# Kernel optimization log

Measured on AMD Instinct MI355X. Metric: run time of the kernel, lower is better.

The kernel has to match this reference:

```python
import jax, jax.numpy as jnp
import numpy as np

N_NODES = 50000
N_EDGES = 800000
IN_DIM = 256
HID = [256, 128]
NEG_SLOPE = 0.01  # F.leaky_relu default


def setup_inputs() -> dict:
    key = jax.random.key(0)
    ks = jax.random.split(key, 8)
    x = jax.random.normal(ks[0], (N_NODES, IN_DIM), dtype=jnp.float32)
    w1 = jax.random.normal(ks[1], (IN_DIM, HID[0]), dtype=jnp.float32) * (1.0 / np.sqrt(IN_DIM))
    b1 = jnp.zeros((HID[0],), dtype=jnp.float32)
    w2 = jax.random.normal(ks[2], (HID[0], HID[1]), dtype=jnp.float32) * (1.0 / np.sqrt(HID[0]))
    b2 = jnp.zeros((HID[1],), dtype=jnp.float32)
    src = jax.random.randint(ks[3], (N_EDGES,), 0, N_NODES, dtype=jnp.int32)
    dst = jax.random.randint(ks[4], (N_EDGES,), 0, N_NODES, dtype=jnp.int32)
    edge_weight = jax.random.uniform(ks[5], (N_EDGES,), dtype=jnp.float32)
    return {"x": x, "w1": w1, "b1": b1, "w2": w2, "b2": b2,
            "src": src, "dst": dst, "edge_weight": edge_weight}


def _gcn_layer(h, w, b, src, dst, ew, n_nodes):
    # GraphConvolution: support = h @ W ; out = spmm(adj, support) + b
    support = h @ w                              # [N, d_out]
    msg = support[src] * ew[:, None]             # [E, d_out] gather + scale
    agg = jax.ops.segment_sum(msg, dst, num_segments=n_nodes)  # [N, d_out]
    return agg + b


def reference(x, w1, b1, w2, b2, src, dst, edge_weight):
    # layer 1: GCN -> leaky_relu -> dropout(eval: identity)
    h = _gcn_layer(x, w1, b1, src, dst, edge_weight, N_NODES)
    h = jax.nn.leaky_relu(h, NEG_SLOPE)
    # layer 2
    h = _gcn_layer(h, w2, b2, src, dst, edge_weight, N_NODES)
    h = jax.nn.leaky_relu(h, NEG_SLOPE)
    return h
```

## Files before the change

kernel.cpp:

```cpp
#include <hip/hip_runtime.h>

#define NEG_SLOPE 0.01f

constexpr int N_NODES_C = 50000;
constexpr int N_EDGES_C = 800000;
constexpr int M_PAD = 50048;
constexpr int META_CAP = 950016;

typedef short bf16x8 __attribute__((ext_vector_type(8)));
typedef float f32x4 __attribute__((ext_vector_type(4)));

__device__ inline unsigned short f2bf(float f) {
  unsigned int u = __float_as_uint(f);
  u += 0x7FFF + ((u >> 16) & 1);
  return (unsigned short)(u >> 16);
}
__device__ inline float bf2f(unsigned int h16) {
  return __uint_as_float(h16 << 16);
}

constexpr int NB_CONVX = (M_PAD * 8) / 256;
constexpr int NB_W1 = (256 * 256) / 256;
constexpr int NB_W2 = (256 * 128) / 256;
constexpr int NB_HIST = ((N_EDGES_C / 4) + 255) / 256;
constexpr int NB_NONH = NB_CONVX + NB_W1 + NB_W2;
constexpr int NB_PRE = NB_NONH + NB_HIST;
constexpr int NB_IL = 2 * NB_HIST;

__global__ __launch_bounds__(256) void pre_kernel(
    const float* __restrict__ x, const float* __restrict__ w1,
    const float* __restrict__ w2, const int* __restrict__ dst,
    unsigned short* __restrict__ xb, unsigned short* __restrict__ w1T,
    unsigned short* __restrict__ w2T, int* __restrict__ counts) {
  const int bx = blockIdx.x;
  const int tid = threadIdx.x;
  int l = 0, isHist = 0, h = 0;
  if (bx < NB_IL) {
    if (bx & 1) { isHist = 1; h = bx >> 1; }
    else l = bx >> 1;
  } else {
    l = bx - NB_HIST;
  }

  if (isHist) {
    int e = (h * 256 + tid) * 4;
    if (e < N_EDGES_C) {
      int4 d4 = *(const int4*)(dst + e);
      atomicAdd(&counts[d4.x], 1);
      atomicAdd(&counts[d4.y], 1);
      atomicAdd(&counts[d4.z], 1);
      atomicAdd(&counts[d4.w], 1);
    }
  } else if (l < NB_CONVX) {
    int idx = l * 256 + tid;
    int row = idx >> 3;
    int c32 = (idx & 7) * 32;
    uint4 o[4];
    if (row < N_NODES_C) {
      const float4* p = (const float4*)(x + (size_t)row * 256 + c32);
      float4 f[8];
#pragma unroll
      for (int i = 0; i < 8; ++i) f[i] = p[i];
#pragma unroll
      for (int i = 0; i < 4; ++i) {
        o[i].x = f2bf(f[2 * i].x) | ((unsigned)f2bf(f[2 * i].y) << 16);
        o[i].y = f2bf(f[2 * i].z) | ((unsigned)f2bf(f[2 * i].w) << 16);
        o[i].z = f2bf(f[2 * i + 1].x) | ((unsigned)f2bf(f[2 * i + 1].y) << 16);
        o[i].w = f2bf(f[2 * i + 1].z) | ((unsigned)f2bf(f[2 * i + 1].w) << 16);
      }
    } else {
#pragma unroll
      for (int i = 0; i < 4; ++i) o[i] = make_uint4(0, 0, 0, 0);
    }
#pragma unroll
    for (int i = 0; i < 4; ++i)
      *(uint4*)(xb + (size_t)row * 256 + c32 + i * 8) = o[i];
  } else if (l < NB_CONVX + NB_W1) {
    int idx = (l - NB_CONVX) * 256 + tid;
    int n = idx >> 8, k = idx & 255;
    w1T[idx] = f2bf(w1[(size_t)k * 256 + n]);
  } else {
    int idx = (l - NB_CONVX - NB_W1) * 256 + tid;
    int n = idx >> 8, k = idx & 255;
    w2T[idx] = f2bf(w2[(size_t)k * 128 + n]);
  }
}

constexpr int NB_NODE = (N_NODES_C + 255) / 256;
constexpr int NB_SCAT = (M_PAD + 255) / 256;

__global__ __launch_bounds__(256) void hist_kernel(const int* __restrict__ counts,
                                                   int* __restrict__ hist2,
                                                   int* __restrict__ ehist) {
  __shared__ int lh[64], le[64];
  const int t = threadIdx.x;
  if (t < 64) { lh[t] = 0; le[t] = 0; }
  __syncthreads();
  const int i = blockIdx.x * 256 + t;
  if (i < N_NODES_C) {
    int d = counts[i];
    int bin = d < 63 ? d : 63;
    atomicAdd(&lh[bin], 1);
    atomicAdd(&le[bin], (d + 3) & ~3);
  }
  __syncthreads();
  if (t < 64) {
    if (lh[t]) atomicAdd(&hist2[t], lh[t]);
    if (le[t]) atomicAdd(&ehist[t], le[t]);
  }
}

__global__ __launch_bounds__(256) void scatter_kernel(
    const int* __restrict__ counts, const int* __restrict__ hist2,
    const int* __restrict__ ehist, int* __restrict__ gclaim_n,
    int* __restrict__ gclaim_e, int* __restrict__ perm,
    int* __restrict__ nstart, int* __restrict__ ndeg,
    int* __restrict__ cursor, unsigned* __restrict__ s_meta) {
  __shared__ int nbase[64], ebase[64], lh[64], le[64], gn[64], ge[64];
  const int t = threadIdx.x;
  if (t < 64) {
    int hv = hist2[t], ev = ehist[t];
    int xs = hv, xe = ev;
#pragma unroll
    for (int off = 1; off < 64; off <<= 1) {
      int a = __shfl_up(xs, off);
      int b = __shfl_up(xe, off);
      if (t >= off) { xs += a; xe += b; }
    }
    nbase[t] = xs - hv;
    ebase[t] = xe - ev;
    lh[t] = 0;
    le[t] = 0;
  }
  __syncthreads();
  const int idx = blockIdx.x * 256 + t;
  int d = -1, bin = 0, lrank = 0, erank = 0;
  if (idx < N_NODES_C) {
    d = counts[idx];
    bin = d < 63 ? d : 63;
    lrank = atomicAdd(&lh[bin], 1);
    erank = atomicAdd(&le[bin], (d + 3) & ~3);
  } else if (idx < M_PAD) {
    perm[idx] = idx;
    nstart[idx] = 0;
    ndeg[idx] = 0;
  }
  __syncthreads();
  if (t < 64) {
    gn[t] = lh[t] ? nbase[t] + atomicAdd(&gclaim_n[t], lh[t]) : 0;
    ge[t] = le[t] ? ebase[t] + atomicAdd(&gclaim_e[t], le[t]) : 0;
  }
  __syncthreads();
  if (d >= 0) {
    const int grank = gn[bin] + lrank;
    const int estart = ge[bin] + erank;
    perm[grank] = idx;
    nstart[grank] = estart;
    ndeg[grank] = d;
    cursor[idx] = estart;
    const int d4 = (d + 3) & ~3;
    for (int j = d; j < d4; ++j) s_meta[estart + j] = 0;
  }
}


#define GLOAD_LDS16(g, l)                                              \
  __builtin_amdgcn_global_load_lds(                                    \
      (__attribute__((address_space(1))) void*)(g),                    \
      (__attribute__((address_space(3))) void*)(l), 16, 0, 0)

__device__ __forceinline__ void gemm_tile(
    const unsigned short* __restrict__ A,
    const unsigned short* __restrict__ BT,
    unsigned short* __restrict__ C,
    int N, int row0, int col0, short* Asm, short* Bsm) {
  constexpr int K = 256;
  const int tid = threadIdx.x;
  const int lane = tid & 63, wave = tid >> 6;
  const int wm = wave & 1, wn = wave >> 1;

  const int ch0 = wave * 2, ch1 = wave * 2 + 1;
  const int o0 = ch0 * 512 + lane * 8;
  const int o1 = ch1 * 512 + lane * 8;
  const int r0 = o0 >> 5, c0 = o0 & 31;
  const int r1 = o1 >> 5, c1 = o1 & 31;

  f32x4 acc[4][4] = {};

  for (int k0 = 0; k0 < K; k0 += 32) {
    GLOAD_LDS16(A + (size_t)(row0 + r0) * K + k0 + c0, &Asm[ch0 * 512]);
    GLOAD_LDS16(A + (size_t)(row0 + r1) * K + k0 + c1, &Asm[ch1 * 512]);
    GLOAD_LDS16(BT + (size_t)(col0 + r0) * K + k0 + c0, &Bsm[ch0 * 512]);
    GLOAD_LDS16(BT + (size_t)(col0 + r1) * K + k0 + c1, &Bsm[ch1 * 512]);
    __builtin_amdgcn_s_waitcnt(0);
    __syncthreads();

    bf16x8 af[4], bf[4];
#pragma unroll
    for (int mt = 0; mt < 4; ++mt)
      af[mt] = *(const bf16x8*)&Asm[(wm * 64 + mt * 16 + (lane & 15)) * 32 + (lane >> 4) * 8];
#pragma unroll
    for (int nt = 0; nt < 4; ++nt)
      bf[nt] = *(const bf16x8*)&Bsm[(wn * 64 + nt * 16 + (lane & 15)) * 32 + (lane >> 4) * 8];
#pragma unroll
    for (int mt = 0; mt < 4; ++mt)
#pragma unroll
      for (int nt = 0; nt < 4; ++nt)
        acc[mt][nt] = __builtin_amdgcn_mfma_f32_16x16x32_bf16(af[mt], bf[nt], acc[mt][nt], 0, 0, 0);
    __syncthreads();
  }

  const int cl = lane & 15, rq = (lane >> 4) * 4;
#pragma unroll
  for (int mt = 0; mt < 4; ++mt) {
    const int rbase = row0 + wm * 64 + mt * 16 + rq;
#pragma unroll
    for (int nt = 0; nt < 4; ++nt) {
      const int col = col0 + wn * 64 + nt * 16 + cl;
      const size_t sbase = ((size_t)(col >> 5) * M_PAD) * 32 + (col & 31);
#pragma unroll
      for (int i = 0; i < 4; ++i)
        C[sbase + (size_t)(rbase + i) * 32] = f2bf(acc[mt][nt][i]);
    }
  }
}

constexpr int NB_GEMM1 = 2 * (M_PAD / 128);
constexpr int NB_FILL = ((N_EDGES_C / 4) + 255) / 256;

__global__ __launch_bounds__(256) void fill_gemm1_kernel(
    const unsigned short* __restrict__ A, const unsigned short* __restrict__ BT,
    unsigned short* __restrict__ C, const int* __restrict__ src,
    const int* __restrict__ dst, const float* __restrict__ ew,
    int* __restrict__ cursor, unsigned* __restrict__ s_meta) {
  __shared__ short Asm[128 * 32];
  __shared__ short Bsm[128 * 32];
  const int b = blockIdx.x;
  if ((b & 1) == 0) {
    const int t = b >> 1;
    gemm_tile(A, BT, C, 256, (t >> 1) * 128, (t & 1) * 128, Asm, Bsm);
  } else {
    const int g = (b >> 1) * 256 + threadIdx.x;
    const int e = g * 4;
    if (e < N_EDGES_C) {
      int4 d4 = *(const int4*)(dst + e);
      int4 s4 = *(const int4*)(src + e);
      float4 w4 = *(const float4*)(ew + e);
      unsigned m0 = (unsigned)s4.x | ((unsigned)f2bf(w4.x) << 16);
      unsigned m1 = (unsigned)s4.y | ((unsigned)f2bf(w4.y) << 16);
      unsigned m2 = (unsigned)s4.z | ((unsigned)f2bf(w4.z) << 16);
      unsigned m3 = (unsigned)s4.w | ((unsigned)f2bf(w4.w) << 16);
      int p0 = atomicAdd(&cursor[d4.x], 1);
      int p1 = atomicAdd(&cursor[d4.y], 1);
      int p2 = atomicAdd(&cursor[d4.z], 1);
      int p3 = atomicAdd(&cursor[d4.w], 1);
      __builtin_nontemporal_store(m0, s_meta + p0);
      __builtin_nontemporal_store(m1, s_meta + p1);
      __builtin_nontemporal_store(m2, s_meta + p2);
      __builtin_nontemporal_store(m3, s_meta + p3);
    }
  }
}

__global__ __launch_bounds__(256) void gemm2_kernel(
    const unsigned short* __restrict__ A, const unsigned short* __restrict__ BT,
    unsigned short* __restrict__ C) {
  __shared__ short Asm[128 * 32];
  __shared__ short Bsm[128 * 32];
  gemm_tile(A, BT, C, 128, blockIdx.x * 128, 0, Asm, Bsm);
}


__device__ inline void fma4(float* acc, uint2 v, float wt) {
  acc[0] += bf2f(v.x & 0xffffu) * wt;
  acc[1] += bf2f(v.x >> 16) * wt;
  acc[2] += bf2f(v.y & 0xffffu) * wt;
  acc[3] += bf2f(v.y >> 16) * wt;
}

__device__ __forceinline__ void gfma4h(float* acc, uint4 m,
                                       const unsigned short* __restrict__ tab,
                                       int dimg) {
  uint2 v0 = *(const uint2*)(tab + (m.x & 0xffffu) * 32 + dimg * 4);
  uint2 v1 = *(const uint2*)(tab + (m.y & 0xffffu) * 32 + dimg * 4);
  uint2 v2 = *(const uint2*)(tab + (m.z & 0xffffu) * 32 + dimg * 4);
  uint2 v3 = *(const uint2*)(tab + (m.w & 0xffffu) * 32 + dimg * 4);
  fma4(acc, v0, bf2f(m.x >> 16));
  fma4(acc, v1, bf2f(m.y >> 16));
  fma4(acc, v2, bf2f(m.z >> 16));
  fma4(acc, v3, bf2f(m.w >> 16));
}

template <int NSLICE, int OUT_D, bool OUT_BF16>
__global__ __launch_bounds__(256) void agg_lite_kernel(
    const unsigned short* __restrict__ supS,
    const unsigned* __restrict__ s_meta,
    const int* __restrict__ nstart, const int* __restrict__ ndeg,
    const int* __restrict__ perm, const float* __restrict__ bias,
    unsigned short* __restrict__ out_bf, float* __restrict__ out_f, int n_total) {
  const int bx = blockIdx.x;
  const int slice = bx & (NSLICE - 1);
  const int group = bx / NSLICE;
  const int tid = threadIdx.x;
  const int wv = tid >> 6;
  const int oct = (tid & 63) >> 3;
  const int dimg = tid & 7;
  const int idx = group * 32 + wv * 8 + oct;
  if (idx >= n_total) return;
  const int n = perm[idx];
  const bool valid = n < N_NODES_C;
  const unsigned short* tab = supS + (size_t)slice * M_PAD * 32;

  float acc[4] = {};
  const int s = nstart[idx];
  const int nq = (ndeg[idx] + 3) >> 2;
  const uint4* mp = (const uint4*)(s_meta + s);

  if (nq > 0) {
    uint4 m0 = mp[0];
    uint4 m1 = (nq > 1) ? mp[1] : make_uint4(0, 0, 0, 0);
    int q = 0;
    for (; q + 2 < nq; q += 2) {
      uint4 p0 = mp[q + 2];
      uint4 p1 = mp[q + 3];
      gfma4h(acc, m0, tab, dimg);
      gfma4h(acc, m1, tab, dimg);
      m0 = p0;
      m1 = p1;
    }
    gfma4h(acc, m0, tab, dimg);
    if (q + 1 < nq) gfma4h(acc, m1, tab, dimg);
  }

  const int dbase = slice * 32 + dimg * 4;
  if (OUT_BF16) {
    unsigned short o[4];
#pragma unroll
    for (int j = 0; j < 4; ++j) {
      if (valid) {
        float v = acc[j] + bias[dbase + j];
        v = v >= 0.f ? v : NEG_SLOPE * v;
        o[j] = f2bf(v);
      } else {
        o[j] = 0;
      }
    }
    uint2 pk;
    pk.x = o[0] | ((unsigned)o[1] << 16);
    pk.y = o[2] | ((unsigned)o[3] << 16);
    *(uint2*)(out_bf + (size_t)n * OUT_D + dbase) = pk;
  } else if (valid) {
    float r[4];
#pragma unroll
    for (int j = 0; j < 4; ++j) {
      float v = acc[j] + bias[dbase + j];
      r[j] = v >= 0.f ? v : NEG_SLOPE * v;
    }
    *(float4*)(out_f + (size_t)n * OUT_D + dbase) = make_float4(r[0], r[1], r[2], r[3]);
  }
}


extern "C" void kernel_launch(void* const* d_in, const int* in_sizes, int n_in,
                              void* d_out, int out_size, void* d_ws, size_t ws_size,
                              hipStream_t stream) {
  const float* x  = (const float*)d_in[0];
  const float* w1 = (const float*)d_in[1];
  const float* b1 = (const float*)d_in[2];
  const float* w2 = (const float*)d_in[3];
  const float* b2 = (const float*)d_in[4];
  const int*   src = (const int*)d_in[5];
  const int*   dst = (const int*)d_in[6];
  const float* ew  = (const float*)d_in[7];
  float* out = (float*)d_out;

  unsigned short* xb   = (unsigned short*)d_ws;
  unsigned short* a2b  = xb + (size_t)M_PAD * 256;
  unsigned short* sup1 = a2b + (size_t)M_PAD * 256;
  unsigned short* sup2 = sup1 + (size_t)M_PAD * 256;
  unsigned short* w1T  = sup2 + (size_t)M_PAD * 128;
  unsigned short* w2T  = w1T + 256 * 256;
  int* counts  = (int*)(w2T + 128 * 256);
  int* cursor  = counts + N_NODES_C;
  int* perm    = cursor + N_NODES_C;
  int* nstart  = perm + M_PAD;
  int* ndeg    = nstart + M_PAD;
  int* hist2   = ndeg + M_PAD;
  int* ehist   = hist2 + 64;
  int* gclaim_n= ehist + 64;
  int* gclaim_e= gclaim_n + 64;
  unsigned* s_meta = (unsigned*)(gclaim_e + 64);

  hipMemsetAsync(counts, 0, N_NODES_C * sizeof(int), stream);
  hipMemsetAsync(hist2, 0, 256 * sizeof(int), stream);
  pre_kernel<<<NB_PRE, 256, 0, stream>>>(x, w1, w2, dst, xb, w1T, w2T, counts);

  hist_kernel<<<NB_NODE, 256, 0, stream>>>(counts, hist2, ehist);
  scatter_kernel<<<NB_SCAT, 256, 0, stream>>>(counts, hist2, ehist, gclaim_n,
                                              gclaim_e, perm, nstart, ndeg,
                                              cursor, s_meta);

  fill_gemm1_kernel<<<NB_GEMM1 + NB_FILL, 256, 0, stream>>>(
      xb, w1T, sup1, src, dst, ew, cursor, s_meta);

  agg_lite_kernel<8, 256, true><<<(M_PAD / 32) * 8, 256, 0, stream>>>(
      sup1, s_meta, nstart, ndeg, perm, b1, a2b, nullptr, M_PAD);

  gemm2_kernel<<<M_PAD / 128, 256, 0, stream>>>(a2b, w2T, sup2);
  agg_lite_kernel<4, 128, false><<<((N_NODES_C + 31) / 32) * 4, 256, 0, stream>>>(
      sup2, s_meta, nstart, ndeg, perm, b2, nullptr, out, N_NODES_C);
}
```

Measured before the change: 284.6 us.

## Switch support to row-major and aggregate with one wave per node

The GEMM epilogues now write the support matrices row-major instead of as 32-column slice tables. The aggregation kernel is rewritten so each 64-lane wave owns one node and gathers whole neighbor rows, with each lane holding 4 columns (layer 1) or 2 columns (layer 2). This reads each node's edge metadata once instead of once per slice and makes every gathered row access wider and contiguous. In exchange it gives up the small per-slice working set that could stay resident in L2, since the gather now touches the full support table.

Result: slower. 296.1 us (+4.0%).

```diff
diff --git a/kernel.cpp b/kernel.cpp
--- a/kernel.cpp
+++ b/kernel.cpp
@@ -173,7 +173,7 @@
     const unsigned short* __restrict__ A,
     const unsigned short* __restrict__ BT,
     unsigned short* __restrict__ C,
-    int N, int row0, int col0, short* Asm, short* Bsm) {
+    int N, int ldc, int row0, int col0, short* Asm, short* Bsm) {
   constexpr int K = 256;
   const int tid = threadIdx.x;
   const int lane = tid & 63, wave = tid >> 6;
@@ -217,10 +217,9 @@
 #pragma unroll
     for (int nt = 0; nt < 4; ++nt) {
       const int col = col0 + wn * 64 + nt * 16 + cl;
-      const size_t sbase = ((size_t)(col >> 5) * M_PAD) * 32 + (col & 31);
 #pragma unroll
       for (int i = 0; i < 4; ++i)
-        C[sbase + (size_t)(rbase + i) * 32] = f2bf(acc[mt][nt][i]);
+        C[(size_t)(rbase + i) * ldc + col] = f2bf(acc[mt][nt][i]);
     }
   }
 }
@@ -238,7 +237,7 @@
   const int b = blockIdx.x;
   if ((b & 1) == 0) {
     const int t = b >> 1;
-    gemm_tile(A, BT, C, 256, (t >> 1) * 128, (t & 1) * 128, Asm, Bsm);
+    gemm_tile(A, BT, C, 256, 256, (t >> 1) * 128, (t & 1) * 128, Asm, Bsm);
   } else {
     const int g = (b >> 1) * 256 + threadIdx.x;
     const int e = g * 4;
@@ -267,54 +266,55 @@
     unsigned short* __restrict__ C) {
   __shared__ short Asm[128 * 32];
   __shared__ short Bsm[128 * 32];
-  gemm_tile(A, BT, C, 128, blockIdx.x * 128, 0, Asm, Bsm);
-}
-
-
-__device__ inline void fma4(float* acc, uint2 v, float wt) {
+  gemm_tile(A, BT, C, 128, 128, blockIdx.x * 128, 0, Asm, Bsm);
+}
+
+
+__device__ __forceinline__ void rfma_256(float* acc, unsigned m,
+                                         const unsigned short* __restrict__ tp) {
+  uint2 v = *(const uint2*)(tp + (size_t)(m & 0xffffu) * 256);
+  float wt = bf2f(m >> 16);
   acc[0] += bf2f(v.x & 0xffffu) * wt;
   acc[1] += bf2f(v.x >> 16) * wt;
   acc[2] += bf2f(v.y & 0xffffu) * wt;
   acc[3] += bf2f(v.y >> 16) * wt;
 }
 
-__device__ __forceinline__ void gfma4h(float* acc, uint4 m,
-                                       const unsigned short* __restrict__ tab,
-                                       int dimg) {
-  uint2 v0 = *(const uint2*)(tab + (m.x & 0xffffu) * 32 + dimg * 4);
-  uint2 v1 = *(const uint2*)(tab + (m.y & 0xffffu) * 32 + dimg * 4);
-  uint2 v2 = *(const uint2*)(tab + (m.z & 0xffffu) * 32 + dimg * 4);
-  uint2 v3 = *(const uint2*)(tab + (m.w & 0xffffu) * 32 + dimg * 4);
-  fma4(acc, v0, bf2f(m.x >> 16));
-  fma4(acc, v1, bf2f(m.y >> 16));
-  fma4(acc, v2, bf2f(m.z >> 16));
-  fma4(acc, v3, bf2f(m.w >> 16));
-}
-
-template <int NSLICE, int OUT_D, bool OUT_BF16>
-__global__ __launch_bounds__(256) void agg_lite_kernel(
-    const unsigned short* __restrict__ supS,
+__device__ __forceinline__ void rfma_128(float* acc, unsigned m,
+                                         const unsigned short* __restrict__ tp) {
+  unsigned v = *(const unsigned*)(tp + (size_t)(m & 0xffffu) * 128);
+  float wt = bf2f(m >> 16);
+  acc[0] += bf2f(v & 0xffffu) * wt;
+  acc[1] += bf2f(v >> 16) * wt;
+}
+
+template <int OUT_D, bool OUT_BF16>
+__global__ __launch_bounds__(256) void agg_row_kernel(
+    const unsigned short* __restrict__ sup,
     const unsigned* __restrict__ s_meta,
     const int* __restrict__ nstart, const int* __restrict__ ndeg,
     const int* __restrict__ perm, const float* __restrict__ bias,
     unsigned short* __restrict__ out_bf, float* __restrict__ out_f, int n_total) {
-  const int bx = blockIdx.x;
-  const int slice = bx & (NSLICE - 1);
-  const int group = bx / NSLICE;
+  constexpr int DPL = OUT_D / 64;
   const int tid = threadIdx.x;
   const int wv = tid >> 6;
-  const int oct = (tid & 63) >> 3;
-  const int dimg = tid & 7;
-  const int idx = group * 32 + wv * 8 + oct;
+  const int lane = tid & 63;
+  const int idx = blockIdx.x * 4 + wv;
   if (idx >= n_total) return;
   const int n = perm[idx];
   const bool valid = n < N_NODES_C;
-  const unsigned short* tab = supS + (size_t)slice * M_PAD * 32;
-
-  float acc[4] = {};
+  const unsigned short* tp = sup + lane * DPL;
+
+  float acc[DPL] = {};
   const int s = nstart[idx];
   const int nq = (ndeg[idx] + 3) >> 2;
   const uint4* mp = (const uint4*)(s_meta + s);
+
+#define RFMA(mm)                              \
+  do {                                        \
+    if (OUT_D == 256) rfma_256(acc, mm, tp);  \
+    else rfma_128(acc, mm, tp);               \
+  } while (0)
 
   if (nq > 0) {
     uint4 m0 = mp[0];
@@ -323,20 +323,21 @@
     for (; q + 2 < nq; q += 2) {
       uint4 p0 = mp[q + 2];
       uint4 p1 = mp[q + 3];
-      gfma4h(acc, m0, tab, dimg);
-      gfma4h(acc, m1, tab, dimg);
+      RFMA(m0.x); RFMA(m0.y); RFMA(m0.z); RFMA(m0.w);
+      RFMA(m1.x); RFMA(m1.y); RFMA(m1.z); RFMA(m1.w);
       m0 = p0;
       m1 = p1;
     }
-    gfma4h(acc, m0, tab, dimg);
-    if (q + 1 < nq) gfma4h(acc, m1, tab, dimg);
-  }
-
-  const int dbase = slice * 32 + dimg * 4;
+    RFMA(m0.x); RFMA(m0.y); RFMA(m0.z); RFMA(m0.w);
+    if (q + 1 < nq) { RFMA(m1.x); RFMA(m1.y); RFMA(m1.z); RFMA(m1.w); }
+  }
+#undef RFMA
+
+  const int dbase = lane * DPL;
   if (OUT_BF16) {
-    unsigned short o[4];
-#pragma unroll
-    for (int j = 0; j < 4; ++j) {
+    unsigned short o[DPL];
+#pragma unroll
+    for (int j = 0; j < DPL; ++j) {
       if (valid) {
         float v = acc[j] + bias[dbase + j];
         v = v >= 0.f ? v : NEG_SLOPE * v;
@@ -350,13 +351,13 @@
     pk.y = o[2] | ((unsigned)o[3] << 16);
     *(uint2*)(out_bf + (size_t)n * OUT_D + dbase) = pk;
   } else if (valid) {
-    float r[4];
-#pragma unroll
-    for (int j = 0; j < 4; ++j) {
+    float r[DPL];
+#pragma unroll
+    for (int j = 0; j < DPL; ++j) {
       float v = acc[j] + bias[dbase + j];
       r[j] = v >= 0.f ? v : NEG_SLOPE * v;
     }
-    *(float4*)(out_f + (size_t)n * OUT_D + dbase) = make_float4(r[0], r[1], r[2], r[3]);
+    *(float2*)(out_f + (size_t)n * OUT_D + dbase) = make_float2(r[0], r[1]);
   }
 }
 
@@ -403,10 +404,10 @@
   fill_gemm1_kernel<<<NB_GEMM1 + NB_FILL, 256, 0, stream>>>(
       xb, w1T, sup1, src, dst, ew, cursor, s_meta);
 
-  agg_lite_kernel<8, 256, true><<<(M_PAD / 32) * 8, 256, 0, stream>>>(
+  agg_row_kernel<256, true><<<M_PAD / 4, 256, 0, stream>>>(
       sup1, s_meta, nstart, ndeg, perm, b1, a2b, nullptr, M_PAD);
 
   gemm2_kernel<<<M_PAD / 128, 256, 0, stream>>>(a2b, w2T, sup2);
-  agg_lite_kernel<4, 128, false><<<((N_NODES_C + 31) / 32) * 4, 256, 0, stream>>>(
+  agg_row_kernel<128, false><<<N_NODES_C / 4, 256, 0, stream>>>(
       sup2, s_meta, nstart, ndeg, perm, b2, nullptr, out, N_NODES_C);
 }
```
